# Performance work log

Measured on AMD Instinct MI355X. Metric: run time of the kernel, lower is better.

Reference implementation:

```python
import jax, jax.numpy as jnp
import numpy as np

N = 50000      # nodes
E = 400000     # edges
IN = 128       # in_dim == emb_dim (residual requires equality)
POS = 64       # pos_in_dim
EMB = 128
LN_EPS = 1e-5


def _ln(x, g, b):
    m = jnp.mean(x, axis=-1, keepdims=True)
    v = jnp.mean((x - m) ** 2, axis=-1, keepdims=True)
    return (x - m) / jnp.sqrt(v + LN_EPS) * g + b


def _gin(x, src, dst, eps, W1, b1, g1, be1, W2, b2):
    # GINConv: mlp((1+eps)*x + sum_{j in N(i)} x_j)
    agg = jax.ops.segment_sum(x[src], dst, num_segments=x.shape[0])
    h = (1.0 + eps) * x + agg
    h = jax.nn.relu(_ln(h @ W1 + b1, g1, be1))
    return h @ W2 + b2


def setup_inputs() -> dict:
    key = jax.random.key(0)
    ks = jax.random.split(key, 8)
    x = jax.random.normal(ks[0], (N, IN), jnp.float32)
    pos = jax.random.normal(ks[1], (N, POS), jnp.float32)
    edge_index = jax.random.randint(ks[2], (2, E), 0, N)
    d = IN + POS
    f32 = jnp.float32
    W1 = (jax.random.normal(ks[3], (d, EMB), f32) / np.sqrt(d))
    W2 = (jax.random.normal(ks[4], (EMB, EMB), f32) / np.sqrt(EMB))
    W1p = (jax.random.normal(ks[5], (POS, EMB), f32) / np.sqrt(POS))
    W2p = (jax.random.normal(ks[6], (EMB, EMB), f32) / np.sqrt(EMB))
    z = jnp.zeros((EMB,), f32)
    o = jnp.ones((EMB,), f32)
    return {
        "x": x, "pos": pos, "edge_index": edge_index,
        "eps": jnp.zeros((), f32), "W1": W1, "b1": z, "g1": o, "be1": z,
        "W2": W2, "b2": z, "ln_g": o, "ln_b": z,
        "epsp": jnp.zeros((), f32), "W1p": W1p, "b1p": z, "g1p": o, "be1p": z,
        "W2p": W2p, "b2p": z, "lnp_g": o, "lnp_b": z,
    }


def reference(x, pos, edge_index, eps, W1, b1, g1, be1, W2, b2, ln_g, ln_b,
              epsp, W1p, b1p, g1p, be1p, W2p, b2p, lnp_g, lnp_b):
    src, dst = edge_index[0], edge_index[1]
    node_feats = jnp.concatenate([x, pos], axis=-1)  # [N, IN+POS]
    h = jax.nn.relu(_ln(_gin(node_feats, src, dst, eps, W1, b1, g1, be1, W2, b2), ln_g, ln_b))
    p = jax.nn.relu(_ln(_gin(pos, src, dst, epsp, W1p, b1p, g1p, be1p, W2p, b2p), lnp_g, lnp_b))
    # dropout is identity in eval mode (model_drop_ratio applied only when training)
    h = h + x  # add_residual=True
    return (h, p)
```

## Files before the change

### kernel.cpp

```cpp
#include <hip/hip_runtime.h>

#define NN    50000
#define NPAD  50048
#define HB    391
#define EE    400000
#define IND   128
#define POSD  64
#define DD    192
#define EMBD  128
#define LNEPS 1e-5f
#define CAP   32

typedef __attribute__((ext_vector_type(8))) short bf16x8;
typedef __attribute__((ext_vector_type(4))) float f32x4;
typedef unsigned short ushort_t;

#define MFMA16 __builtin_amdgcn_mfma_f32_16x16x32_bf16

__device__ inline ushort_t f2bf(float f) {
  union { float f; unsigned u; } v; v.f = f;
  unsigned r = (v.u + 0x7FFFu + ((v.u >> 16) & 1u)) >> 16;
  return (ushort_t)r;
}

__global__ __launch_bounds__(256) void fill_k(
    const int* __restrict__ ei, int* __restrict__ cnt, int* __restrict__ csr) {
  int e = blockIdx.x * 256 + threadIdx.x;
  if (e >= EE) return;
  int src = ei[e];
  int dst = ei[EE + e];
  int idx = atomicAdd(&cnt[dst], 1);
  if (idx < CAP) csr[(size_t)dst * CAP + idx] = src;
}

__global__ __launch_bounds__(256) void wconv_k(
    const float* __restrict__ W1, const float* __restrict__ W2,
    const float* __restrict__ W1p, const float* __restrict__ W2p,
    ushort_t* __restrict__ wt) {
  int tid = blockIdx.x * 256 + threadIdx.x;
  if (tid < 24576) {
    int c = tid / 192, k = tid % 192;
    wt[tid] = f2bf(W1[k * EMBD + c]);
  } else if (tid < 24576 + 16384) {
    int t = tid - 24576; int c = t / 128, k = t % 128;
    wt[tid] = f2bf(W2[k * EMBD + c]);
  } else if (tid < 24576 + 16384 + 8192) {
    int t = tid - 24576 - 16384; int c = t / 64, k = t % 64;
    wt[tid] = f2bf(W1p[k * EMBD + c]);
  } else {
    int t = tid - 24576 - 16384 - 8192; int c = t / 128, k = t % 128;
    wt[tid] = f2bf(W2p[k * EMBD + c]);
  }
}

__global__ __launch_bounds__(256) void gather_k(
    const float* __restrict__ x, const float* __restrict__ pos,
    const int* __restrict__ cnt, const int* __restrict__ csr,
    const float* __restrict__ epsv, const float* __restrict__ epspv,
    ushort_t* __restrict__ h0, ushort_t* __restrict__ p0) {
  const int lane = threadIdx.x & 63;
  const int wv   = threadIdx.x >> 6;
  const int n    = blockIdx.x * 4 + wv;
  if (n >= NPAD) return;

  float a0 = 0.f, a1 = 0.f, a2 = 0.f;
  float xs0 = 0.f, xs1 = 0.f, ps = 0.f;

  if (n < NN) {
    int deg = cnt[n]; if (deg > CAP) deg = CAP;
    const int* row = csr + (size_t)n * CAP;
    int idx = (lane < deg) ? row[lane] : 0;
    int t = 0;
    for (; t + 2 <= deg; t += 2) {
      int s1 = __shfl(idx, t);
      int s2 = __shfl(idx, t + 1);
      float u0 = x[(size_t)s1 * IND + lane];
      float u1 = x[(size_t)s1 * IND + 64 + lane];
      float u2 = pos[(size_t)s1 * POSD + lane];
      float v0 = x[(size_t)s2 * IND + lane];
      float v1 = x[(size_t)s2 * IND + 64 + lane];
      float v2 = pos[(size_t)s2 * POSD + lane];
      a0 += u0 + v0; a1 += u1 + v1; a2 += u2 + v2;
    }
    if (t < deg) {
      int s1 = __shfl(idx, t);
      a0 += x[(size_t)s1 * IND + lane];
      a1 += x[(size_t)s1 * IND + 64 + lane];
      a2 += pos[(size_t)s1 * POSD + lane];
    }
    xs0 = x[(size_t)n * IND + lane];
    xs1 = x[(size_t)n * IND + 64 + lane];
    ps  = pos[(size_t)n * POSD + lane];
  }

  float e1  = 1.0f + epsv[0];
  float ep1 = 1.0f + epspv[0];
  h0[(size_t)n * DD + lane]       = f2bf(fmaf(e1, xs0, a0));
  h0[(size_t)n * DD + 64 + lane]  = f2bf(fmaf(e1, xs1, a1));
  h0[(size_t)n * DD + 128 + lane] = f2bf(fmaf(e1, ps,  a2));
  p0[(size_t)n * POSD + lane]     = f2bf(fmaf(ep1, ps, a2));
}

__device__ inline void ln_epi(f32x4 (&acc)[2][8],
                              const float* __restrict__ bias,
                              const float* __restrict__ gam,
                              const float* __restrict__ bet, int c0) {
  float bv[8], gv[8], bev[8];
#pragma unroll
  for (int nt = 0; nt < 8; ++nt) {
    bv[nt]  = bias[nt * 16 + c0];
    gv[nt]  = gam[nt * 16 + c0];
    bev[nt] = bet[nt * 16 + c0];
  }
#pragma unroll
  for (int mt = 0; mt < 2; ++mt) {
#pragma unroll
    for (int r = 0; r < 4; ++r) {
      float s = 0.f, sq = 0.f;
#pragma unroll
      for (int nt = 0; nt < 8; ++nt) {
        float v = acc[mt][nt][r] + bv[nt];
        acc[mt][nt][r] = v;
        s += v; sq += v * v;
      }
#pragma unroll
      for (int off = 1; off < 16; off <<= 1) {
        s  += __shfl_xor(s, off);
        sq += __shfl_xor(sq, off);
      }
      float mean = s * (1.0f / 128.0f);
      float var  = sq * (1.0f / 128.0f) - mean * mean;
      float rstd = rsqrtf(var + LNEPS);
#pragma unroll
      for (int nt = 0; nt < 8; ++nt) {
        acc[mt][nt][r] =
            fmaxf(fmaf((acc[mt][nt][r] - mean) * rstd, gv[nt], bev[nt]), 0.f);
      }
    }
  }
}

__device__ inline void act_write(char* act, f32x4 (&acc)[2][8], int g, int c0) {
#pragma unroll
  for (int mt = 0; mt < 2; ++mt)
#pragma unroll
    for (int nt = 0; nt < 8; ++nt)
#pragma unroll
      for (int r = 0; r < 4; ++r) {
        int lr   = mt * 16 + g * 4 + r;
        int byte = lr * 256 + (((nt * 16 + c0) * 2) ^ ((lr & 7) << 4));
        *(ushort_t*)(act + byte) = f2bf(acc[mt][nt][r]);
      }
}

__device__ inline void stage_w(const ushort_t* __restrict__ src, char* dst,
                               int rowbytes, int chunks, int tid) {
  int cpr = rowbytes >> 4;
  for (int i = tid; i < chunks; i += 256) {
    int row  = i / cpr;
    int colb = (i - row * cpr) << 4;
    *(bf16x8*)(dst + row * rowbytes + (colb ^ ((row & 7) << 4))) =
        *(const bf16x8*)(src + (size_t)i * 8);
  }
}

__global__ __launch_bounds__(256) void mlp_k(
    const ushort_t* __restrict__ h0, const ushort_t* __restrict__ p0,
    const ushort_t* __restrict__ wt,
    const float* __restrict__ b1, const float* __restrict__ g1,
    const float* __restrict__ be1,
    const float* __restrict__ b2, const float* __restrict__ lng,
    const float* __restrict__ lnb,
    const float* __restrict__ b1p, const float* __restrict__ g1p,
    const float* __restrict__ be1p,
    const float* __restrict__ b2p, const float* __restrict__ lnpg,
    const float* __restrict__ lnpb,
    const float* __restrict__ x, float* __restrict__ out) {
  __shared__ __align__(16) char smem[81920];
  const int tid  = threadIdx.x;
  const int lane = tid & 63;
  const int wv   = tid >> 6;
  const int g    = lane >> 4;
  const int c0   = lane & 15;
  const int bid  = blockIdx.x;
  char* act = smem + 49152 + wv * 8192;

  f32x4 acc[2][8];

  if (bid < HB) {
    const int m0 = bid * 128;
    stage_w(wt, smem, 384, 3072, tid);
    bf16x8 a0[6], a1[6];
    const size_t r0 = (size_t)(m0 + wv * 32 + c0) * DD;
    const size_t r1 = r0 + (size_t)16 * DD;
#pragma unroll
    for (int ks = 0; ks < 6; ++ks) {
      a0[ks] = *(const bf16x8*)(h0 + r0 + ks * 32 + g * 8);
      a1[ks] = *(const bf16x8*)(h0 + r1 + ks * 32 + g * 8);
    }
    __syncthreads();

#pragma unroll
    for (int mt = 0; mt < 2; ++mt)
#pragma unroll
      for (int nt = 0; nt < 8; ++nt) acc[mt][nt] = (f32x4){0.f, 0.f, 0.f, 0.f};
#pragma unroll
    for (int ks = 0; ks < 6; ++ks)
#pragma unroll
      for (int nt = 0; nt < 8; ++nt) {
        int wrow = nt * 16 + c0;
        bf16x8 b = *(const bf16x8*)(smem + wrow * 384 +
                                    ((ks * 64 + g * 16) ^ ((wrow & 7) << 4)));
        acc[0][nt] = MFMA16(a0[ks], b, acc[0][nt], 0, 0, 0);
        acc[1][nt] = MFMA16(a1[ks], b, acc[1][nt], 0, 0, 0);
      }
    ln_epi(acc, b1, g1, be1, c0);
    act_write(act, acc, g, c0);
    __syncthreads();
    stage_w(wt + 24576, smem, 256, 2048, tid);
    __syncthreads();

#pragma unroll
    for (int mt = 0; mt < 2; ++mt)
#pragma unroll
      for (int nt = 0; nt < 8; ++nt) acc[mt][nt] = (f32x4){0.f, 0.f, 0.f, 0.f};
#pragma unroll
    for (int ks = 0; ks < 4; ++ks) {
      bf16x8 am[2];
#pragma unroll
      for (int mt = 0; mt < 2; ++mt) {
        int lr = mt * 16 + c0;
        am[mt] = *(const bf16x8*)(act + lr * 256 +
                                  (((ks * 32 + g * 8) * 2) ^ ((lr & 7) << 4)));
      }
#pragma unroll
      for (int nt = 0; nt < 8; ++nt) {
        int wrow = nt * 16 + c0;
        bf16x8 b = *(const bf16x8*)(smem + wrow * 256 +
                                    ((ks * 64 + g * 16) ^ ((wrow & 7) << 4)));
        acc[0][nt] = MFMA16(am[0], b, acc[0][nt], 0, 0, 0);
        acc[1][nt] = MFMA16(am[1], b, acc[1][nt], 0, 0, 0);
      }
    }
    ln_epi(acc, b2, lng, lnb, c0);
#pragma unroll
    for (int mt = 0; mt < 2; ++mt)
#pragma unroll
      for (int nt = 0; nt < 8; ++nt)
#pragma unroll
        for (int r = 0; r < 4; ++r) {
          int node = m0 + wv * 32 + mt * 16 + g * 4 + r;
          int col  = nt * 16 + c0;
          if (node < NN)
            out[(size_t)node * EMBD + col] =
                acc[mt][nt][r] + x[(size_t)node * IND + col];
        }
  } else {
    const int m0 = (bid - HB) * 128;
    stage_w(wt + 40960, smem, 128, 1024, tid);
    stage_w(wt + 49152, smem + 16384, 256, 2048, tid);
    bf16x8 a0[2], a1[2];
    const size_t r0 = (size_t)(m0 + wv * 32 + c0) * POSD;
    const size_t r1 = r0 + (size_t)16 * POSD;
#pragma unroll
    for (int ks = 0; ks < 2; ++ks) {
      a0[ks] = *(const bf16x8*)(p0 + r0 + ks * 32 + g * 8);
      a1[ks] = *(const bf16x8*)(p0 + r1 + ks * 32 + g * 8);
    }
    __syncthreads();

#pragma unroll
    for (int mt = 0; mt < 2; ++mt)
#pragma unroll
      for (int nt = 0; nt < 8; ++nt) acc[mt][nt] = (f32x4){0.f, 0.f, 0.f, 0.f};
#pragma unroll
    for (int ks = 0; ks < 2; ++ks)
#pragma unroll
      for (int nt = 0; nt < 8; ++nt) {
        int wrow = nt * 16 + c0;
        bf16x8 b = *(const bf16x8*)(smem + wrow * 128 +
                                    ((ks * 64 + g * 16) ^ ((wrow & 7) << 4)));
        acc[0][nt] = MFMA16(a0[ks], b, acc[0][nt], 0, 0, 0);
        acc[1][nt] = MFMA16(a1[ks], b, acc[1][nt], 0, 0, 0);
      }
    ln_epi(acc, b1p, g1p, be1p, c0);
    act_write(act, acc, g, c0);

#pragma unroll
    for (int mt = 0; mt < 2; ++mt)
#pragma unroll
      for (int nt = 0; nt < 8; ++nt) acc[mt][nt] = (f32x4){0.f, 0.f, 0.f, 0.f};
#pragma unroll
    for (int ks = 0; ks < 4; ++ks) {
      bf16x8 am[2];
#pragma unroll
      for (int mt = 0; mt < 2; ++mt) {
        int lr = mt * 16 + c0;
        am[mt] = *(const bf16x8*)(act + lr * 256 +
                                  (((ks * 32 + g * 8) * 2) ^ ((lr & 7) << 4)));
      }
#pragma unroll
      for (int nt = 0; nt < 8; ++nt) {
        int wrow = nt * 16 + c0;
        bf16x8 b = *(const bf16x8*)(smem + 16384 + wrow * 256 +
                                    ((ks * 64 + g * 16) ^ ((wrow & 7) << 4)));
        acc[0][nt] = MFMA16(am[0], b, acc[0][nt], 0, 0, 0);
        acc[1][nt] = MFMA16(am[1], b, acc[1][nt], 0, 0, 0);
      }
    }
    ln_epi(acc, b2p, lnpg, lnpb, c0);
#pragma unroll
    for (int mt = 0; mt < 2; ++mt)
#pragma unroll
      for (int nt = 0; nt < 8; ++nt)
#pragma unroll
        for (int r = 0; r < 4; ++r) {
          int node = m0 + wv * 32 + mt * 16 + g * 4 + r;
          int col  = nt * 16 + c0;
          if (node < NN)
            out[(size_t)NN * EMBD + (size_t)node * EMBD + col] = acc[mt][nt][r];
        }
  }
}

extern "C" void kernel_launch(void* const* d_in, const int* in_sizes, int n_in,
                              void* d_out, int out_size, void* d_ws, size_t ws_size,
                              hipStream_t stream) {
  const float* x    = (const float*)d_in[0];
  const float* pos  = (const float*)d_in[1];
  const int*   ei   = (const int*)d_in[2];
  const float* eps  = (const float*)d_in[3];
  const float* W1   = (const float*)d_in[4];
  const float* b1   = (const float*)d_in[5];
  const float* g1   = (const float*)d_in[6];
  const float* be1  = (const float*)d_in[7];
  const float* W2   = (const float*)d_in[8];
  const float* b2   = (const float*)d_in[9];
  const float* lng  = (const float*)d_in[10];
  const float* lnb  = (const float*)d_in[11];
  const float* epsp = (const float*)d_in[12];
  const float* W1p  = (const float*)d_in[13];
  const float* b1p  = (const float*)d_in[14];
  const float* g1p  = (const float*)d_in[15];
  const float* be1p = (const float*)d_in[16];
  const float* W2p  = (const float*)d_in[17];
  const float* b2p  = (const float*)d_in[18];
  const float* lnpg = (const float*)d_in[19];
  const float* lnpb = (const float*)d_in[20];

  char* ws = (char*)d_ws;
  int*      cnt = (int*)ws;
  int*      csr = (int*)(ws + 200000);
  ushort_t* h0  = (ushort_t*)(ws + 6600000);
  ushort_t* p0  = (ushort_t*)(ws + 25818432);
  ushort_t* wt  = (ushort_t*)(ws + 32224576);
  float*    out = (float*)d_out;

  hipMemsetAsync(cnt, 0, (size_t)NN * sizeof(int), stream);
  fill_k<<<(EE + 255) / 256, 256, 0, stream>>>(ei, cnt, csr);
  wconv_k<<<256, 256, 0, stream>>>(W1, W2, W1p, W2p, wt);
  gather_k<<<NPAD / 4, 256, 0, stream>>>(x, pos, cnt, csr, eps, epsp, h0, p0);
  mlp_k<<<2 * HB, 256, 0, stream>>>(
      h0, p0, wt, b1, g1, be1, b2, lng, lnb,
      b1p, g1p, be1p, b2p, lnpg, lnpb, x, out);
}
```

Measured before the change: 126.2 us.

## Fuse neighbor gather into MLP kernel and pre-convert features to bf16

Result: slower. 228.7 us (+81.2%).

```diff
diff --git a/kernel.cpp b/kernel.cpp
--- a/kernel.cpp
+++ b/kernel.cpp
@@ -11,9 +11,15 @@
 #define LNEPS 1e-5f
 #define CAP   32
 
+#define PREP_B 4692
+#define FILL_B 1563
+#define WC_B   256
+
 typedef __attribute__((ext_vector_type(8))) short bf16x8;
+typedef __attribute__((ext_vector_type(4))) unsigned short u16x4;
 typedef __attribute__((ext_vector_type(4))) float f32x4;
 typedef unsigned short ushort_t;
+typedef unsigned int uint_t;
 
 #define MFMA16 __builtin_amdgcn_mfma_f32_16x16x32_bf16
 
@@ -22,83 +28,59 @@
   unsigned r = (v.u + 0x7FFFu + ((v.u >> 16) & 1u)) >> 16;
   return (ushort_t)r;
 }
-
-__global__ __launch_bounds__(256) void fill_k(
-    const int* __restrict__ ei, int* __restrict__ cnt, int* __restrict__ csr) {
-  int e = blockIdx.x * 256 + threadIdx.x;
-  if (e >= EE) return;
-  int src = ei[e];
-  int dst = ei[EE + e];
-  int idx = atomicAdd(&cnt[dst], 1);
-  if (idx < CAP) csr[(size_t)dst * CAP + idx] = src;
-}
-
-__global__ __launch_bounds__(256) void wconv_k(
+__device__ inline float bf2f(unsigned u) {
+  union { unsigned u; float f; } v; v.u = u << 16;
+  return v.f;
+}
+
+__global__ __launch_bounds__(256) void prep_k(
+    const float* __restrict__ x, const float* __restrict__ pos,
+    const int* __restrict__ ei,
     const float* __restrict__ W1, const float* __restrict__ W2,
     const float* __restrict__ W1p, const float* __restrict__ W2p,
-    ushort_t* __restrict__ wt) {
-  int tid = blockIdx.x * 256 + threadIdx.x;
-  if (tid < 24576) {
-    int c = tid / 192, k = tid % 192;
-    wt[tid] = f2bf(W1[k * EMBD + c]);
-  } else if (tid < 24576 + 16384) {
-    int t = tid - 24576; int c = t / 128, k = t % 128;
-    wt[tid] = f2bf(W2[k * EMBD + c]);
-  } else if (tid < 24576 + 16384 + 8192) {
-    int t = tid - 24576 - 16384; int c = t / 64, k = t % 64;
-    wt[tid] = f2bf(W1p[k * EMBD + c]);
+    int* __restrict__ cnt, int* __restrict__ csr,
+    ushort_t* __restrict__ cat, ushort_t* __restrict__ wt) {
+  const int bid = blockIdx.x;
+  if (bid < PREP_B) {
+    int id  = bid * 256 + threadIdx.x;
+    int n   = id / 24, sub = id - n * 24;
+    bf16x8 o = (bf16x8){0, 0, 0, 0, 0, 0, 0, 0};
+    if (n < NN) {
+      const float* src = (sub < 16) ? (x + (size_t)n * IND + sub * 8)
+                                    : (pos + (size_t)n * POSD + (sub - 16) * 8);
+      f32x4 v0 = *(const f32x4*)(src);
+      f32x4 v1 = *(const f32x4*)(src + 4);
+#pragma unroll
+      for (int i = 0; i < 4; ++i) {
+        o[i]     = (short)f2bf(v0[i]);
+        o[i + 4] = (short)f2bf(v1[i]);
+      }
+    }
+    *(bf16x8*)(cat + (size_t)n * DD + sub * 8) = o;
+  } else if (bid < PREP_B + FILL_B) {
+    int e = (bid - PREP_B) * 256 + threadIdx.x;
+    if (e < EE) {
+      int src = ei[e];
+      int dst = ei[EE + e];
+      int idx = atomicAdd(&cnt[dst], 1);
+      if (idx < CAP) csr[(size_t)dst * CAP + idx] = src;
+    }
   } else {
-    int t = tid - 24576 - 16384 - 8192; int c = t / 128, k = t % 128;
-    wt[tid] = f2bf(W2p[k * EMBD + c]);
+    int t = (bid - PREP_B - FILL_B) * 256 + threadIdx.x;
+    if (t < 24576) {
+      int c = t / 192, k = t % 192;
+      wt[t] = f2bf(W1[k * EMBD + c]);
+    } else if (t < 40960) {
+      int q = t - 24576; int c = q / 128, k = q % 128;
+      wt[t] = f2bf(W2[k * EMBD + c]);
+    } else if (t < 49152) {
+      int q = t - 40960; int c = q / 64, k = q % 64;
+      wt[t] = f2bf(W1p[k * EMBD + c]);
+    } else {
+      int q = t - 49152; int c = q / 128, k = q % 128;
+      wt[t] = f2bf(W2p[k * EMBD + c]);
+    }
   }
-}
-
-__global__ __launch_bounds__(256) void gather_k(
-    const float* __restrict__ x, const float* __restrict__ pos,
-    const int* __restrict__ cnt, const int* __restrict__ csr,
-    const float* __restrict__ epsv, const float* __restrict__ epspv,
-    ushort_t* __restrict__ h0, ushort_t* __restrict__ p0) {
-  const int lane = threadIdx.x & 63;
-  const int wv   = threadIdx.x >> 6;
-  const int n    = blockIdx.x * 4 + wv;
-  if (n >= NPAD) return;
-
-  float a0 = 0.f, a1 = 0.f, a2 = 0.f;
-  float xs0 = 0.f, xs1 = 0.f, ps = 0.f;
-
-  if (n < NN) {
-    int deg = cnt[n]; if (deg > CAP) deg = CAP;
-    const int* row = csr + (size_t)n * CAP;
-    int idx = (lane < deg) ? row[lane] : 0;
-    int t = 0;
-    for (; t + 2 <= deg; t += 2) {
-      int s1 = __shfl(idx, t);
-      int s2 = __shfl(idx, t + 1);
-      float u0 = x[(size_t)s1 * IND + lane];
-      float u1 = x[(size_t)s1 * IND + 64 + lane];
-      float u2 = pos[(size_t)s1 * POSD + lane];
-      float v0 = x[(size_t)s2 * IND + lane];
-      float v1 = x[(size_t)s2 * IND + 64 + lane];
-      float v2 = pos[(size_t)s2 * POSD + lane];
-      a0 += u0 + v0; a1 += u1 + v1; a2 += u2 + v2;
-    }
-    if (t < deg) {
-      int s1 = __shfl(idx, t);
-      a0 += x[(size_t)s1 * IND + lane];
-      a1 += x[(size_t)s1 * IND + 64 + lane];
-      a2 += pos[(size_t)s1 * POSD + lane];
-    }
-    xs0 = x[(size_t)n * IND + lane];
-    xs1 = x[(size_t)n * IND + 64 + lane];
-    ps  = pos[(size_t)n * POSD + lane];
-  }
-
-  float e1  = 1.0f + epsv[0];
-  float ep1 = 1.0f + epspv[0];
-  h0[(size_t)n * DD + lane]       = f2bf(fmaf(e1, xs0, a0));
-  h0[(size_t)n * DD + 64 + lane]  = f2bf(fmaf(e1, xs1, a1));
-  h0[(size_t)n * DD + 128 + lane] = f2bf(fmaf(e1, ps,  a2));
-  p0[(size_t)n * POSD + lane]     = f2bf(fmaf(ep1, ps, a2));
 }
 
 __device__ inline void ln_epi(f32x4 (&acc)[2][8],
@@ -165,12 +147,14 @@
 }
 
 __global__ __launch_bounds__(256) void mlp_k(
-    const ushort_t* __restrict__ h0, const ushort_t* __restrict__ p0,
-    const ushort_t* __restrict__ wt,
+    const ushort_t* __restrict__ cat, const int* __restrict__ cnt,
+    const int* __restrict__ csr, const ushort_t* __restrict__ wt,
+    const float* __restrict__ epsv,
     const float* __restrict__ b1, const float* __restrict__ g1,
     const float* __restrict__ be1,
     const float* __restrict__ b2, const float* __restrict__ lng,
     const float* __restrict__ lnb,
+    const float* __restrict__ epspv,
     const float* __restrict__ b1p, const float* __restrict__ g1p,
     const float* __restrict__ be1p,
     const float* __restrict__ b2p, const float* __restrict__ lnpg,
@@ -189,15 +173,60 @@
 
   if (bid < HB) {
     const int m0 = bid * 128;
+    const float e1 = 1.0f + epsv[0];
+
+    for (int j = 0; j < 32; ++j) {
+      int n = m0 + wv * 32 + j;
+      int deg = 0;
+      if (n < NN) { deg = cnt[n]; if (deg > CAP) deg = CAP; }
+      int idx = 0;
+      if (lane < deg) idx = csr[(size_t)n * CAP + lane];
+      float a0 = 0.f, a1 = 0.f, a2 = 0.f, a3 = 0.f;
+      int t = 0;
+      for (; t + 4 <= deg; t += 4) {
+        int s1 = __shfl(idx, t),     s2 = __shfl(idx, t + 1);
+        int s3 = __shfl(idx, t + 2), s4 = __shfl(idx, t + 3);
+        if (lane < 48) {
+          u16x4 u1 = *(const u16x4*)(cat + (size_t)s1 * DD + lane * 4);
+          u16x4 u2 = *(const u16x4*)(cat + (size_t)s2 * DD + lane * 4);
+          u16x4 u3 = *(const u16x4*)(cat + (size_t)s3 * DD + lane * 4);
+          u16x4 u4 = *(const u16x4*)(cat + (size_t)s4 * DD + lane * 4);
+          a0 += (bf2f(u1[0]) + bf2f(u2[0])) + (bf2f(u3[0]) + bf2f(u4[0]));
+          a1 += (bf2f(u1[1]) + bf2f(u2[1])) + (bf2f(u3[1]) + bf2f(u4[1]));
+          a2 += (bf2f(u1[2]) + bf2f(u2[2])) + (bf2f(u3[2]) + bf2f(u4[2]));
+          a3 += (bf2f(u1[3]) + bf2f(u2[3])) + (bf2f(u3[3]) + bf2f(u4[3]));
+        }
+      }
+      for (; t < deg; ++t) {
+        int s1 = __shfl(idx, t);
+        if (lane < 48) {
+          u16x4 u = *(const u16x4*)(cat + (size_t)s1 * DD + lane * 4);
+          a0 += bf2f(u[0]); a1 += bf2f(u[1]); a2 += bf2f(u[2]); a3 += bf2f(u[3]);
+        }
+      }
+      if (lane < 48) {
+        u16x4 sv = *(const u16x4*)(cat + (size_t)n * DD + lane * 4);
+        u16x4 o;
+        o[0] = f2bf(fmaf(e1, bf2f(sv[0]), a0));
+        o[1] = f2bf(fmaf(e1, bf2f(sv[1]), a1));
+        o[2] = f2bf(fmaf(e1, bf2f(sv[2]), a2));
+        o[3] = f2bf(fmaf(e1, bf2f(sv[3]), a3));
+        int row = wv * 32 + j;
+        *(u16x4*)(smem + row * 384 + ((lane * 8) ^ ((j & 7) << 4))) = o;
+      }
+    }
+
+    bf16x8 a0r[6], a1r[6];
+#pragma unroll
+    for (int ks = 0; ks < 6; ++ks) {
+      int r0 = wv * 32 + c0;
+      a0r[ks] = *(const bf16x8*)(smem + r0 * 384 +
+                                 ((ks * 64 + g * 16) ^ ((c0 & 7) << 4)));
+      a1r[ks] = *(const bf16x8*)(smem + (r0 + 16) * 384 +
+                                 ((ks * 64 + g * 16) ^ ((c0 & 7) << 4)));
+    }
+    __syncthreads();
     stage_w(wt, smem, 384, 3072, tid);
-    bf16x8 a0[6], a1[6];
-    const size_t r0 = (size_t)(m0 + wv * 32 + c0) * DD;
-    const size_t r1 = r0 + (size_t)16 * DD;
-#pragma unroll
-    for (int ks = 0; ks < 6; ++ks) {
-      a0[ks] = *(const bf16x8*)(h0 + r0 + ks * 32 + g * 8);
-      a1[ks] = *(const bf16x8*)(h0 + r1 + ks * 32 + g * 8);
-    }
     __syncthreads();
 
 #pragma unroll
@@ -211,8 +240,8 @@
         int wrow = nt * 16 + c0;
         bf16x8 b = *(const bf16x8*)(smem + wrow * 384 +
                                     ((ks * 64 + g * 16) ^ ((wrow & 7) << 4)));
-        acc[0][nt] = MFMA16(a0[ks], b, acc[0][nt], 0, 0, 0);
-        acc[1][nt] = MFMA16(a1[ks], b, acc[1][nt], 0, 0, 0);
+        acc[0][nt] = MFMA16(a0r[ks], b, acc[0][nt], 0, 0, 0);
+        acc[1][nt] = MFMA16(a1r[ks], b, acc[1][nt], 0, 0, 0);
       }
     ln_epi(acc, b1, g1, be1, c0);
     act_write(act, acc, g, c0);
@@ -257,16 +286,49 @@
         }
   } else {
     const int m0 = (bid - HB) * 128;
+    const float ep1 = 1.0f + epspv[0];
+    const int half = lane >> 5, l2 = lane & 31;
+
+    for (int j = 0; j < 32; j += 2) {
+      int n = m0 + wv * 32 + j + half;
+      int deg = 0;
+      if (n < NN) { deg = cnt[n]; if (deg > CAP) deg = CAP; }
+      int idx = 0;
+      if (l2 < deg) idx = csr[(size_t)n * CAP + l2];
+      int dm = max(__shfl(deg, 0), __shfl(deg, 32));
+      float a0 = 0.f, a1 = 0.f;
+      for (int t = 0; t < dm; t += 2) {
+        int s1 = __shfl(idx, half * 32 + t);
+        int s2 = __shfl(idx, half * 32 + t + 1);
+        if (t < deg) {
+          uint_t u = *(const uint_t*)(cat + (size_t)s1 * DD + 128 + l2 * 2);
+          a0 += bf2f(u & 0xffffu); a1 += bf2f(u >> 16);
+        }
+        if (t + 1 < deg) {
+          uint_t u = *(const uint_t*)(cat + (size_t)s2 * DD + 128 + l2 * 2);
+          a0 += bf2f(u & 0xffffu); a1 += bf2f(u >> 16);
+        }
+      }
+      uint_t sv = *(const uint_t*)(cat + (size_t)n * DD + 128 + l2 * 2);
+      float v0 = fmaf(ep1, bf2f(sv & 0xffffu), a0);
+      float v1 = fmaf(ep1, bf2f(sv >> 16), a1);
+      int r = wv * 32 + j + half;
+      uint_t o = (uint_t)f2bf(v0) | ((uint_t)f2bf(v1) << 16);
+      *(uint_t*)(smem + r * 128 + ((l2 * 4) ^ ((r & 7) << 4))) = o;
+    }
+
+    bf16x8 a0r[2], a1r[2];
+#pragma unroll
+    for (int ks = 0; ks < 2; ++ks) {
+      int r0 = wv * 32 + c0;
+      a0r[ks] = *(const bf16x8*)(smem + r0 * 128 +
+                                 ((ks * 64 + g * 16) ^ ((c0 & 7) << 4)));
+      a1r[ks] = *(const bf16x8*)(smem + (r0 + 16) * 128 +
+                                 ((ks * 64 + g * 16) ^ ((c0 & 7) << 4)));
+    }
+    __syncthreads();
     stage_w(wt + 40960, smem, 128, 1024, tid);
     stage_w(wt + 49152, smem + 16384, 256, 2048, tid);
-    bf16x8 a0[2], a1[2];
-    const size_t r0 = (size_t)(m0 + wv * 32 + c0) * POSD;
-    const size_t r1 = r0 + (size_t)16 * POSD;
-#pragma unroll
-    for (int ks = 0; ks < 2; ++ks) {
-      a0[ks] = *(const bf16x8*)(p0 + r0 + ks * 32 + g * 8);
-      a1[ks] = *(const bf16x8*)(p0 + r1 + ks * 32 + g * 8);
-    }
     __syncthreads();
 
 #pragma unroll
@@ -280,8 +342,8 @@
         int wrow = nt * 16 + c0;
         bf16x8 b = *(const bf16x8*)(smem + wrow * 128 +
                                     ((ks * 64 + g * 16) ^ ((wrow & 7) << 4)));
-        acc[0][nt] = MFMA16(a0[ks], b, acc[0][nt], 0, 0, 0);
-        acc[1][nt] = MFMA16(a1[ks], b, acc[1][nt], 0, 0, 0);
+        acc[0][nt] = MFMA16(a0r[ks], b, acc[0][nt], 0, 0, 0);
+        acc[1][nt] = MFMA16(a1r[ks], b, acc[1][nt], 0, 0, 0);
       }
     ln_epi(acc, b1p, g1p, be1p, c0);
     act_write(act, acc, g, c0);
@@ -351,16 +413,14 @@
   char* ws = (char*)d_ws;
   int*      cnt = (int*)ws;
   int*      csr = (int*)(ws + 200000);
-  ushort_t* h0  = (ushort_t*)(ws + 6600000);
-  ushort_t* p0  = (ushort_t*)(ws + 25818432);
-  ushort_t* wt  = (ushort_t*)(ws + 32224576);
+  ushort_t* cat = (ushort_t*)(ws + 6600000);
+  ushort_t* wt  = (ushort_t*)(ws + 25818432);
   float*    out = (float*)d_out;
 
   hipMemsetAsync(cnt, 0, (size_t)NN * sizeof(int), stream);
-  fill_k<<<(EE + 255) / 256, 256, 0, stream>>>(ei, cnt, csr);
-  wconv_k<<<256, 256, 0, stream>>>(W1, W2, W1p, W2p, wt);
-  gather_k<<<NPAD / 4, 256, 0, stream>>>(x, pos, cnt, csr, eps, epsp, h0, p0);
+  prep_k<<<PREP_B + FILL_B + WC_B, 256, 0, stream>>>(
+      x, pos, ei, W1, W2, W1p, W2p, cnt, csr, cat, wt);
   mlp_k<<<2 * HB, 256, 0, stream>>>(
-      h0, p0, wt, b1, g1, be1, b2, lng, lnb,
-      b1p, g1p, be1p, b2p, lnpg, lnpb, x, out);
-}
+      cat, cnt, csr, wt, eps, b1, g1, be1, b2, lng, lnb,
+      epsp, b1p, g1p, be1p, b2p, lnpg, lnpb, x, out);
+}
```

## Pre-convert node features to bf16 and gather half-width rows with fused prep kernel

Applied to the files above, without the earlier changes.

After: 116.6 us. -7.6%, faster.

```diff
diff --git a/kernel.cpp b/kernel.cpp
--- a/kernel.cpp
+++ b/kernel.cpp
@@ -11,9 +11,15 @@
 #define LNEPS 1e-5f
 #define CAP   32
 
+#define PREP_B 4692
+#define FILL_B 1563
+#define WC_B   256
+
 typedef __attribute__((ext_vector_type(8))) short bf16x8;
+typedef __attribute__((ext_vector_type(4))) unsigned short u16x4;
 typedef __attribute__((ext_vector_type(4))) float f32x4;
 typedef unsigned short ushort_t;
+typedef unsigned int uint_t;
 
 #define MFMA16 __builtin_amdgcn_mfma_f32_16x16x32_bf16
 
@@ -21,6 +27,60 @@
   union { float f; unsigned u; } v; v.f = f;
   unsigned r = (v.u + 0x7FFFu + ((v.u >> 16) & 1u)) >> 16;
   return (ushort_t)r;
+}
+__device__ inline float bf2f(unsigned u) {
+  union { unsigned u; float f; } v; v.u = u << 16;
+  return v.f;
+}
+
+__global__ __launch_bounds__(256) void prep_k(
+    const float* __restrict__ x, const float* __restrict__ pos,
+    const int* __restrict__ ei,
+    const float* __restrict__ W1, const float* __restrict__ W2,
+    const float* __restrict__ W1p, const float* __restrict__ W2p,
+    int* __restrict__ cnt, int* __restrict__ csr,
+    ushort_t* __restrict__ cat, ushort_t* __restrict__ wt) {
+  const int bid = blockIdx.x;
+  if (bid < PREP_B) {
+    int id  = bid * 256 + threadIdx.x;
+    int n   = id / 24, sub = id - n * 24;
+    bf16x8 o = (bf16x8){0, 0, 0, 0, 0, 0, 0, 0};
+    if (n < NN) {
+      const float* src = (sub < 16) ? (x + (size_t)n * IND + sub * 8)
+                                    : (pos + (size_t)n * POSD + (sub - 16) * 8);
+      f32x4 v0 = *(const f32x4*)(src);
+      f32x4 v1 = *(const f32x4*)(src + 4);
+#pragma unroll
+      for (int i = 0; i < 4; ++i) {
+        o[i]     = (short)f2bf(v0[i]);
+        o[i + 4] = (short)f2bf(v1[i]);
+      }
+    }
+    *(bf16x8*)(cat + (size_t)n * DD + sub * 8) = o;
+  } else if (bid < PREP_B + FILL_B) {
+    int e = (bid - PREP_B) * 256 + threadIdx.x;
+    if (e < EE) {
+      int src = ei[e];
+      int dst = ei[EE + e];
+      int idx = atomicAdd(&cnt[dst], 1);
+      if (idx < CAP) csr[(size_t)dst * CAP + idx] = src;
+    }
+  } else {
+    int t = (bid - PREP_B - FILL_B) * 256 + threadIdx.x;
+    if (t < 24576) {
+      int c = t / 192, k = t % 192;
+      wt[t] = f2bf(W1[k * EMBD + c]);
+    } else if (t < 40960) {
+      int q = t - 24576; int c = q / 128, k = q % 128;
+      wt[t] = f2bf(W2[k * EMBD + c]);
+    } else if (t < 49152) {
+      int q = t - 40960; int c = q / 64, k = q % 64;
+      wt[t] = f2bf(W1p[k * EMBD + c]);
+    } else {
+      int q = t - 49152; int c = q / 128, k = q % 128;
+      wt[t] = f2bf(W2p[k * EMBD + c]);
+    }
+  }
 }
 
 __global__ __launch_bounds__(256) void fill_k(
@@ -41,14 +101,14 @@
   if (tid < 24576) {
     int c = tid / 192, k = tid % 192;
     wt[tid] = f2bf(W1[k * EMBD + c]);
-  } else if (tid < 24576 + 16384) {
+  } else if (tid < 40960) {
     int t = tid - 24576; int c = t / 128, k = t % 128;
     wt[tid] = f2bf(W2[k * EMBD + c]);
-  } else if (tid < 24576 + 16384 + 8192) {
-    int t = tid - 24576 - 16384; int c = t / 64, k = t % 64;
+  } else if (tid < 49152) {
+    int t = tid - 40960; int c = t / 64, k = t % 64;
     wt[tid] = f2bf(W1p[k * EMBD + c]);
   } else {
-    int t = tid - 24576 - 16384 - 8192; int c = t / 128, k = t % 128;
+    int t = tid - 49152; int c = t / 128, k = t % 128;
     wt[tid] = f2bf(W2p[k * EMBD + c]);
   }
 }
@@ -99,6 +159,71 @@
   h0[(size_t)n * DD + 64 + lane]  = f2bf(fmaf(e1, xs1, a1));
   h0[(size_t)n * DD + 128 + lane] = f2bf(fmaf(e1, ps,  a2));
   p0[(size_t)n * POSD + lane]     = f2bf(fmaf(ep1, ps, a2));
+}
+
+__global__ __launch_bounds__(256) void gather2_k(
+    const ushort_t* __restrict__ cat, const int* __restrict__ cnt,
+    const int* __restrict__ csr,
+    const float* __restrict__ epsv, const float* __restrict__ epspv,
+    ushort_t* __restrict__ h0, ushort_t* __restrict__ p0) {
+  const int lane = threadIdx.x & 63;
+  const int wv   = threadIdx.x >> 6;
+  const int half = lane >> 5;
+  const int l2   = lane & 31;
+  const int n    = blockIdx.x * 8 + wv * 2 + half;
+
+  int deg = 0;
+  if (n < NN) { deg = cnt[n]; if (deg > CAP) deg = CAP; }
+  int idx = (l2 < deg) ? csr[(size_t)n * CAP + l2] : 0;
+
+  float a0 = 0.f, a1 = 0.f, a2 = 0.f, a3 = 0.f, a4 = 0.f, a5 = 0.f;
+  int t = 0;
+  for (; t + 2 <= deg; t += 2) {
+    int s1 = __shfl(idx, half * 32 + t);
+    int s2 = __shfl(idx, half * 32 + t + 1);
+    const ushort_t* r1 = cat + (size_t)s1 * DD;
+    const ushort_t* r2 = cat + (size_t)s2 * DD;
+    u16x4 u1 = *(const u16x4*)(r1 + l2 * 4);
+    uint_t v1 = *(const uint_t*)(r1 + 128 + l2 * 2);
+    u16x4 u2 = *(const u16x4*)(r2 + l2 * 4);
+    uint_t v2 = *(const uint_t*)(r2 + 128 + l2 * 2);
+    a0 += bf2f(u1[0]) + bf2f(u2[0]);
+    a1 += bf2f(u1[1]) + bf2f(u2[1]);
+    a2 += bf2f(u1[2]) + bf2f(u2[2]);
+    a3 += bf2f(u1[3]) + bf2f(u2[3]);
+    a4 += bf2f(v1 & 0xffffu) + bf2f(v2 & 0xffffu);
+    a5 += bf2f(v1 >> 16) + bf2f(v2 >> 16);
+  }
+  if (t < deg) {
+    int s1 = __shfl(idx, half * 32 + t);
+    const ushort_t* r1 = cat + (size_t)s1 * DD;
+    u16x4 u1 = *(const u16x4*)(r1 + l2 * 4);
+    uint_t v1 = *(const uint_t*)(r1 + 128 + l2 * 2);
+    a0 += bf2f(u1[0]); a1 += bf2f(u1[1]);
+    a2 += bf2f(u1[2]); a3 += bf2f(u1[3]);
+    a4 += bf2f(v1 & 0xffffu); a5 += bf2f(v1 >> 16);
+  }
+
+  const float e1  = 1.0f + epsv[0];
+  const float ep1 = 1.0f + epspv[0];
+  const ushort_t* self = cat + (size_t)n * DD;
+  u16x4 su = *(const u16x4*)(self + l2 * 4);
+  uint_t sv = *(const uint_t*)(self + 128 + l2 * 2);
+
+  u16x4 o;
+  o[0] = f2bf(fmaf(e1, bf2f(su[0]), a0));
+  o[1] = f2bf(fmaf(e1, bf2f(su[1]), a1));
+  o[2] = f2bf(fmaf(e1, bf2f(su[2]), a2));
+  o[3] = f2bf(fmaf(e1, bf2f(su[3]), a3));
+  *(u16x4*)(h0 + (size_t)n * DD + l2 * 4) = o;
+
+  float p4 = bf2f(sv & 0xffffu), p5 = bf2f(sv >> 16);
+  uint_t oh = (uint_t)f2bf(fmaf(e1, p4, a4)) |
+              ((uint_t)f2bf(fmaf(e1, p5, a5)) << 16);
+  *(uint_t*)(h0 + (size_t)n * DD + 128 + l2 * 2) = oh;
+  uint_t op = (uint_t)f2bf(fmaf(ep1, p4, a4)) |
+              ((uint_t)f2bf(fmaf(ep1, p5, a5)) << 16);
+  *(uint_t*)(p0 + (size_t)n * POSD + l2 * 2) = op;
 }
 
 __device__ inline void ln_epi(f32x4 (&acc)[2][8],
@@ -349,18 +474,39 @@
   const float* lnpb = (const float*)d_in[20];
 
   char* ws = (char*)d_ws;
-  int*      cnt = (int*)ws;
-  int*      csr = (int*)(ws + 200000);
-  ushort_t* h0  = (ushort_t*)(ws + 6600000);
-  ushort_t* p0  = (ushort_t*)(ws + 25818432);
-  ushort_t* wt  = (ushort_t*)(ws + 32224576);
-  float*    out = (float*)d_out;
+  float* out = (float*)d_out;
+
+  const size_t CATB = (size_t)NPAD * DD * 2;
+  const size_t P0B  = (size_t)NPAD * POSD * 2;
+  const size_t NEED_BIG = 200000 + 6400000 + CATB + CATB + P0B + 131072;
+
+  int* cnt = (int*)ws;
+  int* csr = (int*)(ws + 200000);
 
   hipMemsetAsync(cnt, 0, (size_t)NN * sizeof(int), stream);
-  fill_k<<<(EE + 255) / 256, 256, 0, stream>>>(ei, cnt, csr);
-  wconv_k<<<256, 256, 0, stream>>>(W1, W2, W1p, W2p, wt);
-  gather_k<<<NPAD / 4, 256, 0, stream>>>(x, pos, cnt, csr, eps, epsp, h0, p0);
-  mlp_k<<<2 * HB, 256, 0, stream>>>(
-      h0, p0, wt, b1, g1, be1, b2, lng, lnb,
-      b1p, g1p, be1p, b2p, lnpg, lnpb, x, out);
-}
+
+  if (ws_size >= NEED_BIG) {
+    ushort_t* cat = (ushort_t*)(ws + 6600000);
+    ushort_t* h0  = (ushort_t*)(ws + 6600000 + CATB);
+    ushort_t* p0  = (ushort_t*)(ws + 6600000 + 2 * CATB);
+    ushort_t* wt  = (ushort_t*)(ws + 6600000 + 2 * CATB + P0B);
+
+    prep_k<<<PREP_B + FILL_B + WC_B, 256, 0, stream>>>(
+        x, pos, ei, W1, W2, W1p, W2p, cnt, csr, cat, wt);
+    gather2_k<<<NPAD / 8, 256, 0, stream>>>(cat, cnt, csr, eps, epsp, h0, p0);
+    mlp_k<<<2 * HB, 256, 0, stream>>>(
+        h0, p0, wt, b1, g1, be1, b2, lng, lnb,
+        b1p, g1p, be1p, b2p, lnpg, lnpb, x, out);
+  } else {
+    ushort_t* h0 = (ushort_t*)(ws + 6600000);
+    ushort_t* p0 = (ushort_t*)(ws + 6600000 + CATB);
+    ushort_t* wt = (ushort_t*)(ws + 6600000 + CATB + P0B);
+
+    fill_k<<<(EE + 255) / 256, 256, 0, stream>>>(ei, cnt, csr);
+    wconv_k<<<256, 256, 0, stream>>>(W1, W2, W1p, W2p, wt);
+    gather_k<<<NPAD / 4, 256, 0, stream>>>(x, pos, cnt, csr, eps, epsp, h0, p0);
+    mlp_k<<<2 * HB, 256, 0, stream>>>(
+        h0, p0, wt, b1, g1, be1, b2, lng, lnb,
+        b1p, g1p, be1p, b2p, lnpg, lnpb, x, out);
+  }
+}
```
